# Performance work log

Hardware: AMD Instinct MI355X
Metric: run time of the kernel (lower is better)

## Reference

```python
import jax, jax.numpy as jnp
import numpy as np

N = 100000
E = 1600000
D = 64
N_LAYERS = 2


def setup_inputs() -> dict:
    key = jax.random.key(0)
    ks = jax.random.split(key, 4 + 4 * N_LAYERS)
    h = jax.random.normal(ks[0], (N, D), dtype=jnp.float32)
    x = jax.random.normal(ks[1], (N, 3), dtype=jnp.float32)
    edge_index = jax.random.randint(ks[2], (2, E), 0, N, dtype=jnp.int64)
    node_mask = jnp.ones((N, 1), dtype=jnp.float32)
    scale = 1.0 / np.sqrt(D)
    params = {}
    for i in range(N_LAYERS):
        params[f'W1_{i}'] = jax.random.normal(ks[4 + 4 * i], (D, D), dtype=jnp.float32) * scale
        params[f'b1_{i}'] = jax.random.normal(ks[5 + 4 * i], (D,), dtype=jnp.float32) * scale
        params[f'W2_{i}'] = jax.random.normal(ks[6 + 4 * i], (D, D), dtype=jnp.float32) * scale
        params[f'b2_{i}'] = jax.random.normal(ks[7 + 4 * i], (D,), dtype=jnp.float32) * scale
    return dict(h=h, x=x, edge_index=edge_index, node_mask=node_mask, **params)


def _gin_layer(h, src, dst, W1, b1, W2, b2):
    # GINConv with eps=0: mlp(h_i + sum_{j->i} h_j)
    agg = jax.ops.segment_sum(h[src], dst, num_segments=N)  # [N, D]
    z = h + agg
    z = jax.nn.relu(z @ W1 + b1)
    return z @ W2 + b2


def reference(h, x, edge_index, node_mask,
              W1_0, b1_0, W2_0, b2_0,
              W1_1, b1_1, W2_1, b2_1):
    src, dst = edge_index[0], edge_index[1]
    h = _gin_layer(h, src, dst, W1_0, b1_0, W2_0, b2_0)
    h = _gin_layer(h, src, dst, W1_1, b1_1, W2_1, b2_1)
    h = h * node_mask
    return (h, x)
```

## Files before the change

### kernel.cpp

```cpp
#include <hip/hip_runtime.h>


#define NN 100000
#define EE 1600000
#define CAP 48
#define NBIN 1024
#define CHB 6250
#define OVF_CAPN 8000

#define OVFC_OFF   1024
#define OVF_OFF    1026
#define BSTART_OFF 17056
#define CURSOR_OFF 18112
#define CNT_OFF    19200
#define BUCK_OFF   119296
#define BINNED_OFF 4919296
#define HB_OFF     4919296
#define PW_OFF     8119328

typedef __attribute__((ext_vector_type(8))) short s8v;
typedef __attribute__((ext_vector_type(4))) float f4v;

union U8 { unsigned u[4]; s8v s; };

static __device__ __forceinline__ unsigned short f2bf(float f) {
  unsigned u = __float_as_uint(f);
  return (unsigned short)((u + 0x7FFF + ((u >> 16) & 1)) >> 16);
}
static __device__ __forceinline__ float bf2f(unsigned short s) {
  return __uint_as_float(((unsigned)s) << 16);
}
static __device__ __forceinline__ unsigned pk2(float lo, float hi) {
  return (unsigned)f2bf(lo) | ((unsigned)f2bf(hi) << 16);
}

__global__ __launch_bounds__(256) void setup_k(const float* __restrict__ W1a,
                                               const float* __restrict__ W2a,
                                               const float* __restrict__ W1b,
                                               const float* __restrict__ W2b,
                                               unsigned short* __restrict__ pw,
                                               int* __restrict__ wsp) {
  const int t = threadIdx.x;
#pragma unroll
  for (int i = t; i < 2048; i += 256) wsp[i] = 0;
  const float* Ws[4] = {W1a, W2a, W1b, W2b};
#pragma unroll
  for (int m = 0; m < 4; ++m) {
    const float* __restrict__ W = Ws[m];
#pragma unroll 1
    for (int i = 0; i < 16; ++i) {
      const int e = i * 256 + t;
      const int j = e & 7;
      const int lv = (e >> 3) & 63;
      const int ks = (e >> 9) & 1;
      const int tt = e >> 10;
      const int k = ks * 32 + (lv >> 4) * 8 + j;
      const int n = tt * 16 + (lv & 15);
      pw[m * 4096 + e] = f2bf(W[k * 64 + n]);
    }
  }
}

__global__ __launch_bounds__(256) void hist_k(const int* __restrict__ dst,
                                              int* __restrict__ binTot) {
  __shared__ int hist[NBIN];
  const int t = threadIdx.x;
#pragma unroll
  for (int b = t; b < NBIN; b += 256) hist[b] = 0;
  __syncthreads();
  const int s = blockIdx.x * CHB;
#pragma unroll 1
  for (int p = t; p < CHB / 2; p += 256) {
    const int2 dd = *reinterpret_cast<const int2*>(dst + s + 2 * p);
    atomicAdd(&hist[dd.x >> 7], 1);
    atomicAdd(&hist[dd.y >> 7], 1);
  }
  __syncthreads();
#pragma unroll
  for (int b = t; b < NBIN; b += 256) {
    const int c = hist[b];
    if (c) atomicAdd(&binTot[b], c);
  }
}

__global__ __launch_bounds__(1024) void scan_k(const int* __restrict__ binTot,
                                               int* __restrict__ binStart,
                                               int* __restrict__ cursor) {
  __shared__ int sh[NBIN];
  const int t = threadIdx.x;
  const int v = binTot[t];
  sh[t] = v;
  __syncthreads();
  for (int off = 1; off < NBIN; off <<= 1) {
    const int x = (t >= off) ? sh[t - off] : 0;
    __syncthreads();
    sh[t] += x;
    __syncthreads();
  }
  binStart[t] = sh[t] - v;
  cursor[t] = sh[t] - v;
  if (t == NBIN - 1) binStart[NBIN] = sh[t];
}

__global__ __launch_bounds__(256) void scatter_k(const int* __restrict__ src,
                                                 const int* __restrict__ dst,
                                                 int* __restrict__ cursor,
                                                 int* __restrict__ binned) {
  __shared__ int hist[NBIN], base[NBIN], lcnt[NBIN];
  const int t = threadIdx.x;
#pragma unroll
  for (int b = t; b < NBIN; b += 256) { hist[b] = 0; lcnt[b] = 0; }
  __syncthreads();
  const int s = blockIdx.x * CHB;
#pragma unroll 1
  for (int p = t; p < CHB / 2; p += 256) {
    const int2 dd = *reinterpret_cast<const int2*>(dst + s + 2 * p);
    atomicAdd(&hist[dd.x >> 7], 1);
    atomicAdd(&hist[dd.y >> 7], 1);
  }
  __syncthreads();
#pragma unroll
  for (int b = t; b < NBIN; b += 256) {
    const int c = hist[b];
    base[b] = c ? atomicAdd(&cursor[b], c) : 0;
  }
  __syncthreads();
#pragma unroll 1
  for (int p = t; p < CHB / 2; p += 256) {
    const int i = s + 2 * p;
    const int2 dd = *reinterpret_cast<const int2*>(dst + i);
    const int2 ss = *reinterpret_cast<const int2*>(src + i);
    int bin = dd.x >> 7;
    int off = atomicAdd(&lcnt[bin], 1);
    binned[base[bin] + off] = ((dd.x & 127) << 17) | ss.x;
    bin = dd.y >> 7;
    off = atomicAdd(&lcnt[bin], 1);
    binned[base[bin] + off] = ((dd.y & 127) << 17) | ss.y;
  }
}

__global__ __launch_bounds__(256) void bucketize_k(const int* __restrict__ binStart,
                                                   const int* __restrict__ binned,
                                                   int* __restrict__ bucket,
                                                   int* __restrict__ cnt,
                                                   int* __restrict__ ovf) {
  __shared__ int c128[128];
  const int t = threadIdx.x;
  const int bin = blockIdx.x;
  const int nbase = bin << 7;
  if (t < 128) c128[t] = 0;
  __syncthreads();
  const int s0 = binStart[bin], s1 = binStart[bin + 1];
#pragma unroll 1
  for (int i = s0 + t; i < s1; i += 256) {
    const int p = binned[i];
    const int dlow = p >> 17;
    const int sv = p & 131071;
    const int slot = atomicAdd(&c128[dlow], 1);
    if (slot < CAP) {
      bucket[(nbase + dlow) * CAP + slot] = sv;
    } else {
      const int q = atomicAdd(&ovf[-2], 1);
      if (q < OVF_CAPN) { ovf[2 * q] = nbase + dlow; ovf[2 * q + 1] = sv; }
    }
  }
  __syncthreads();
  if (t < 128 && nbase + t < NN) {
    const int dc = min(c128[t], CAP);
    cnt[nbase + t] = c128[t];
    const int pad = min((dc + 15) & ~15, CAP);
    int* __restrict__ brow = bucket + (nbase + t) * CAP;
#pragma unroll 1
    for (int q2 = dc; q2 < pad; ++q2) brow[q2] = NN;
  }
}

__global__ __launch_bounds__(256) void cvtx_k(const float* __restrict__ h,
                                              unsigned* __restrict__ hb,
                                              const float* __restrict__ x,
                                              float* __restrict__ ox) {
  const int b = blockIdx.x;
  const int t = threadIdx.x;
  if (b < 3125) {
    const int i = b * 256 + t;
    const float4* __restrict__ h4 = reinterpret_cast<const float4*>(h);
    const float4 a = h4[2 * i], c = h4[2 * i + 1];
    uint4 o;
    o.x = pk2(a.x, a.y); o.y = pk2(a.z, a.w);
    o.z = pk2(c.x, c.y); o.w = pk2(c.z, c.w);
    reinterpret_cast<uint4*>(hb)[i] = o;
  } else {
    if (b == 3125 && t < 32) hb[NN * 32 + t] = 0;
    const int i = (b - 3125) * 256 + t;
    if (i < (NN * 3) / 4)
      reinterpret_cast<float4*>(ox)[i] = reinterpret_cast<const float4*>(x)[i];
  }
}

__global__ __launch_bounds__(256) void agg_k(const unsigned short* __restrict__ hb,
                                             const int* __restrict__ cnt,
                                             const int* __restrict__ bucket,
                                             unsigned* __restrict__ zbu) {
  const int l = threadIdx.x & 63;
  const int s = l >> 4, g = l & 15;
  int n = blockIdx.x * 4 + (threadIdx.x >> 6);
  n = __builtin_amdgcn_readfirstlane(n);
  if (n >= NN) return;
  const int deg = min(cnt[n], CAP);
  const int nit = (deg + 15) >> 4;
  const int4* __restrict__ brow4 = reinterpret_cast<const int4*>(bucket + n * CAP);
  const uint2* __restrict__ h2 = reinterpret_cast<const uint2*>(hb);

  const uint2 sv = h2[n * 16 + g];
  const unsigned m0 = (s == 0) ? sv.x : 0u;
  const unsigned m1 = (s == 0) ? sv.y : 0u;
  float a0 = __uint_as_float(m0 << 16);
  float a1 = __uint_as_float(m0 & 0xffff0000u);
  float a2 = __uint_as_float(m1 << 16);
  float a3 = __uint_as_float(m1 & 0xffff0000u);

#pragma unroll 1
  for (int it = 0; it < nit; ++it) {
    const int4 q = brow4[it * 4 + s];
    const uint2 v0 = h2[q.x * 16 + g];
    const uint2 v1 = h2[q.y * 16 + g];
    const uint2 v2 = h2[q.z * 16 + g];
    const uint2 v3 = h2[q.w * 16 + g];
#define ACCU(vv)                                   \
    a0 += __uint_as_float(vv.x << 16);             \
    a1 += __uint_as_float(vv.x & 0xffff0000u);     \
    a2 += __uint_as_float(vv.y << 16);             \
    a3 += __uint_as_float(vv.y & 0xffff0000u);
    ACCU(v0) ACCU(v1) ACCU(v2) ACCU(v3)
#undef ACCU
  }

  a0 += __shfl_xor(a0, 16); a1 += __shfl_xor(a1, 16);
  a2 += __shfl_xor(a2, 16); a3 += __shfl_xor(a3, 16);
  a0 += __shfl_xor(a0, 32); a1 += __shfl_xor(a1, 32);
  a2 += __shfl_xor(a2, 32); a3 += __shfl_xor(a3, 32);

  if (s == 0) {
    uint2 o;
    o.x = pk2(a0, a1);
    o.y = pk2(a2, a3);
    reinterpret_cast<uint2*>(zbu)[n * 32 + g] = o;
  }
}

__global__ __launch_bounds__(256) void ovf_fix_k(const unsigned short* __restrict__ hb,
                                                 char* __restrict__ zb,
                                                 const int* __restrict__ ovfCnt,
                                                 const int* __restrict__ ovf) {
  const int cv = min(ovfCnt[0], OVF_CAPN);
  const int l = threadIdx.x & 63;
  const int w = threadIdx.x >> 6;
  for (int p = w; p < cv; p += 4) {
    const int d = ovf[2 * p];
    const int s = ovf[2 * p + 1];
    const float add = bf2f(hb[(s << 6) | l]);
    unsigned* wp = reinterpret_cast<unsigned*>(zb + d * 256 + (l >> 1) * 4);
    const bool hi = l & 1;
    unsigned cur = atomicAdd(wp, 0u);
    while (true) {
      const unsigned short hv = hi ? (unsigned short)(cur >> 16) : (unsigned short)(cur & 0xffffu);
      const unsigned short nh = f2bf(bf2f(hv) + add);
      const unsigned nw = hi ? ((cur & 0x0000ffffu) | ((unsigned)nh << 16))
                             : ((cur & 0xffff0000u) | (unsigned)nh);
      const unsigned prev = atomicCAS(wp, cur, nw);
      if (prev == cur) break;
      cur = prev;
    }
  }
}

template <int OUTBF>
__global__ __launch_bounds__(256) void mlp_mfma_k(
    const char* __restrict__ zb,
    void* __restrict__ hout,
    const unsigned short* __restrict__ pw1, const float* __restrict__ b1,
    const unsigned short* __restrict__ pw2, const float* __restrict__ b2,
    const float* __restrict__ mask) {
  __shared__ unsigned ldsu[128 * 33];
  const int tid = threadIdx.x;
  const int w = tid >> 6, l = tid & 63, g = l >> 4, mi = l & 15;
  const int m0 = blockIdx.x * 128;
  const int rbase = w * 32;

  s8v zf[2][2];
#pragma unroll
  for (int tm = 0; tm < 2; ++tm) {
    const int node = m0 + rbase + tm * 16 + mi;
    const int nc = node < NN ? node : NN - 1;
#pragma unroll
    for (int ks = 0; ks < 2; ++ks)
      zf[tm][ks] = *reinterpret_cast<const s8v*>(zb + nc * 256 + (ks * 32 + g * 8) * 2);
  }

  f4v acc[4][2];
#pragma unroll
  for (int t = 0; t < 4; ++t) {
    const f4v bv = *reinterpret_cast<const f4v*>(b1 + t * 16 + g * 4);
    acc[t][0] = bv; acc[t][1] = bv;
  }
#pragma unroll
  for (int t = 0; t < 4; ++t) {
#pragma unroll
    for (int ks = 0; ks < 2; ++ks) {
      const s8v wf = *reinterpret_cast<const s8v*>(pw1 + ((t * 2 + ks) * 64 + l) * 8);
#pragma unroll
      for (int tm = 0; tm < 2; ++tm)
        acc[t][tm] = __builtin_amdgcn_mfma_f32_16x16x32_bf16(wf, zf[tm][ks], acc[t][tm], 0, 0, 0);
    }
  }

#pragma unroll
  for (int t = 0; t < 4; ++t) {
#pragma unroll
    for (int tm = 0; tm < 2; ++tm) {
      const f4v a = acc[t][tm];
      const int row = rbase + tm * 16 + mi;
      const int base = row * 33 + t * 8 + g * 2;
      ldsu[base]     = pk2(fmaxf(a.x, 0.f), fmaxf(a.y, 0.f));
      ldsu[base + 1] = pk2(fmaxf(a.z, 0.f), fmaxf(a.w, 0.f));
    }
  }
  __syncthreads();

  s8v cf[2][2];
#pragma unroll
  for (int tm = 0; tm < 2; ++tm) {
    const int row = rbase + tm * 16 + mi;
#pragma unroll
    for (int ks = 0; ks < 2; ++ks) {
      const int b0 = row * 33 + ks * 16 + g * 4;
      U8 u8;
      u8.u[0] = ldsu[b0 + 0];
      u8.u[1] = ldsu[b0 + 1];
      u8.u[2] = ldsu[b0 + 2];
      u8.u[3] = ldsu[b0 + 3];
      cf[tm][ks] = u8.s;
    }
  }

  f4v acc2[4][2];
#pragma unroll
  for (int t = 0; t < 4; ++t) {
    const f4v bv = *reinterpret_cast<const f4v*>(b2 + t * 16 + g * 4);
    acc2[t][0] = bv; acc2[t][1] = bv;
  }
#pragma unroll
  for (int t = 0; t < 4; ++t) {
#pragma unroll
    for (int ks = 0; ks < 2; ++ks) {
      const s8v wf = *reinterpret_cast<const s8v*>(pw2 + ((t * 2 + ks) * 64 + l) * 8);
#pragma unroll
      for (int tm = 0; tm < 2; ++tm)
        acc2[t][tm] = __builtin_amdgcn_mfma_f32_16x16x32_bf16(wf, cf[tm][ks], acc2[t][tm], 0, 0, 0);
    }
  }

  if (OUTBF) {
    unsigned* __restrict__ ho = reinterpret_cast<unsigned*>(hout);
#pragma unroll
    for (int tm = 0; tm < 2; ++tm) {
      const int node = m0 + rbase + tm * 16 + mi;
      if (node < NN) {
#pragma unroll
        for (int t = 0; t < 4; ++t) {
          const f4v a = acc2[t][tm];
          const int idx = node * 32 + t * 8 + g * 2;
          uint2 p;
          p.x = pk2(a.x, a.y);
          p.y = pk2(a.z, a.w);
          *reinterpret_cast<uint2*>(&ho[idx]) = p;
        }
      }
    }
  } else {
    float* __restrict__ fo = reinterpret_cast<float*>(hout);
#pragma unroll
    for (int tm = 0; tm < 2; ++tm) {
      const int node = m0 + rbase + tm * 16 + mi;
      if (node < NN) {
        const float mv = mask[node];
#pragma unroll
        for (int t = 0; t < 4; ++t) {
          f4v v = acc2[t][tm];
          v *= mv;
          *reinterpret_cast<f4v*>(fo + node * 64 + t * 16 + g * 4) = v;
        }
      }
    }
  }
}

extern "C" void kernel_launch(void* const* d_in, const int* in_sizes, int n_in,
                              void* d_out, int out_size, void* d_ws, size_t ws_size,
                              hipStream_t stream) {
  (void)in_sizes; (void)n_in; (void)out_size; (void)ws_size;
  const float* h    = (const float*)d_in[0];
  const float* x    = (const float*)d_in[1];
  const int*   ei   = (const int*)d_in[2];
  const float* mask = (const float*)d_in[3];
  const float* W1_0 = (const float*)d_in[4];
  const float* b1_0 = (const float*)d_in[5];
  const float* W2_0 = (const float*)d_in[6];
  const float* b2_0 = (const float*)d_in[7];
  const float* W1_1 = (const float*)d_in[8];
  const float* b1_1 = (const float*)d_in[9];
  const float* W2_1 = (const float*)d_in[10];
  const float* b2_1 = (const float*)d_in[11];
  float* out = (float*)d_out;

  const int* src = ei;
  const int* dst = ei + EE;

  int* wsp       = (int*)d_ws;
  int* binTot    = wsp;
  int* ovfCnt    = wsp + OVFC_OFF;
  int* ovf       = wsp + OVF_OFF;
  int* binStart  = wsp + BSTART_OFF;
  int* cursor    = wsp + CURSOR_OFF;
  int* cnt       = wsp + CNT_OFF;
  int* bucket    = wsp + BUCK_OFF;
  int* binned    = wsp + BINNED_OFF;
  unsigned* hb   = (unsigned*)(wsp + HB_OFF);
  unsigned short* pw = (unsigned short*)(wsp + PW_OFF);
  const unsigned short* hbs = (const unsigned short*)hb;
  unsigned* zbu  = (unsigned*)d_out;
  char* zb       = (char*)d_out;

  setup_k<<<1, 256, 0, stream>>>(W1_0, W2_0, W1_1, W2_1, pw, wsp);
  hist_k<<<256, 256, 0, stream>>>(dst, binTot);
  scan_k<<<1, 1024, 0, stream>>>(binTot, binStart, cursor);
  scatter_k<<<256, 256, 0, stream>>>(src, dst, cursor, binned);
  bucketize_k<<<782, 256, 0, stream>>>(binStart, binned, bucket, cnt, ovf);

  cvtx_k<<<3418, 256, 0, stream>>>(h, hb, x, out + NN * 64);

  agg_k<<<25000, 256, 0, stream>>>(hbs, cnt, bucket, zbu);
  ovf_fix_k<<<1, 256, 0, stream>>>(hbs, zb, ovfCnt, ovf);
  mlp_mfma_k<1><<<782, 256, 0, stream>>>(zb, hb, pw, b1_0, pw + 4096, b2_0, nullptr);

  agg_k<<<25000, 256, 0, stream>>>(hbs, cnt, bucket, zbu);
  ovf_fix_k<<<1, 256, 0, stream>>>(hbs, zb, ovfCnt, ovf);
  mlp_mfma_k<0><<<782, 256, 0, stream>>>(zb, out, pw + 8192, b1_1, pw + 12288, b2_1, mask);
}
```

Measured before the change: 164.4 us.

## Use fixed-capacity bins to drop histogram/scan passes; process two nodes per wave in aggregation

Edge binning now gives each destination bin a fixed-capacity region, so the separate histogram and scan kernels are removed. Edges that overflow a bin go to the existing overflow list. The aggregation kernel also handles two destination nodes per wavefront, which puts more independent gathers in flight and halves the grid size. The cost is extra register pressure, and correctness now depends on the overflow path whenever a bin exceeds its capacity.

Result: faster. 146.1 us (-11.1%).

```diff
diff --git a/kernel.cpp b/kernel.cpp
--- a/kernel.cpp
+++ b/kernel.cpp
@@ -5,13 +5,12 @@
 #define EE 1600000
 #define CAP 48
 #define NBIN 1024
+#define BINCAP 2688
 #define CHB 6250
 #define OVF_CAPN 8000
 
 #define OVFC_OFF   1024
 #define OVF_OFF    1026
-#define BSTART_OFF 17056
-#define CURSOR_OFF 18112
 #define CNT_OFF    19200
 #define BUCK_OFF   119296
 #define BINNED_OFF 4919296
@@ -42,7 +41,8 @@
                                                int* __restrict__ wsp) {
   const int t = threadIdx.x;
 #pragma unroll
-  for (int i = t; i < 2048; i += 256) wsp[i] = 0;
+  for (int i = t; i < NBIN; i += 256) wsp[i] = i * BINCAP;
+  if (t == 0) wsp[OVFC_OFF] = 0;
   const float* Ws[4] = {W1a, W2a, W1b, W2b};
 #pragma unroll
   for (int m = 0; m < 4; ++m) {
@@ -61,12 +61,15 @@
   }
 }
 
-__global__ __launch_bounds__(256) void hist_k(const int* __restrict__ dst,
-                                              int* __restrict__ binTot) {
-  __shared__ int hist[NBIN];
+__global__ __launch_bounds__(256) void scatter_k(const int* __restrict__ src,
+                                                 const int* __restrict__ dst,
+                                                 int* __restrict__ gcur,
+                                                 int* __restrict__ binned,
+                                                 int* __restrict__ ovf) {
+  __shared__ int hist[NBIN], base[NBIN], lcnt[NBIN];
   const int t = threadIdx.x;
 #pragma unroll
-  for (int b = t; b < NBIN; b += 256) hist[b] = 0;
+  for (int b = t; b < NBIN; b += 256) { hist[b] = 0; lcnt[b] = 0; }
   __syncthreads();
   const int s = blockIdx.x * CHB;
 #pragma unroll 1
@@ -79,50 +82,7 @@
 #pragma unroll
   for (int b = t; b < NBIN; b += 256) {
     const int c = hist[b];
-    if (c) atomicAdd(&binTot[b], c);
-  }
-}
-
-__global__ __launch_bounds__(1024) void scan_k(const int* __restrict__ binTot,
-                                               int* __restrict__ binStart,
-                                               int* __restrict__ cursor) {
-  __shared__ int sh[NBIN];
-  const int t = threadIdx.x;
-  const int v = binTot[t];
-  sh[t] = v;
-  __syncthreads();
-  for (int off = 1; off < NBIN; off <<= 1) {
-    const int x = (t >= off) ? sh[t - off] : 0;
-    __syncthreads();
-    sh[t] += x;
-    __syncthreads();
-  }
-  binStart[t] = sh[t] - v;
-  cursor[t] = sh[t] - v;
-  if (t == NBIN - 1) binStart[NBIN] = sh[t];
-}
-
-__global__ __launch_bounds__(256) void scatter_k(const int* __restrict__ src,
-                                                 const int* __restrict__ dst,
-                                                 int* __restrict__ cursor,
-                                                 int* __restrict__ binned) {
-  __shared__ int hist[NBIN], base[NBIN], lcnt[NBIN];
-  const int t = threadIdx.x;
-#pragma unroll
-  for (int b = t; b < NBIN; b += 256) { hist[b] = 0; lcnt[b] = 0; }
-  __syncthreads();
-  const int s = blockIdx.x * CHB;
-#pragma unroll 1
-  for (int p = t; p < CHB / 2; p += 256) {
-    const int2 dd = *reinterpret_cast<const int2*>(dst + s + 2 * p);
-    atomicAdd(&hist[dd.x >> 7], 1);
-    atomicAdd(&hist[dd.y >> 7], 1);
-  }
-  __syncthreads();
-#pragma unroll
-  for (int b = t; b < NBIN; b += 256) {
-    const int c = hist[b];
-    base[b] = c ? atomicAdd(&cursor[b], c) : 0;
+    base[b] = c ? atomicAdd(&gcur[b], c) : 0;
   }
   __syncthreads();
 #pragma unroll 1
@@ -130,16 +90,30 @@
     const int i = s + 2 * p;
     const int2 dd = *reinterpret_cast<const int2*>(dst + i);
     const int2 ss = *reinterpret_cast<const int2*>(src + i);
-    int bin = dd.x >> 7;
-    int off = atomicAdd(&lcnt[bin], 1);
-    binned[base[bin] + off] = ((dd.x & 127) << 17) | ss.x;
-    bin = dd.y >> 7;
-    off = atomicAdd(&lcnt[bin], 1);
-    binned[base[bin] + off] = ((dd.y & 127) << 17) | ss.y;
-  }
-}
-
-__global__ __launch_bounds__(256) void bucketize_k(const int* __restrict__ binStart,
+    {
+      const int bin = dd.x >> 7;
+      const int slot = base[bin] + atomicAdd(&lcnt[bin], 1);
+      if (slot < (bin + 1) * BINCAP) {
+        binned[slot] = ((dd.x & 127) << 17) | ss.x;
+      } else {
+        const int q = atomicAdd(&ovf[-2], 1);
+        if (q < OVF_CAPN) { ovf[2 * q] = dd.x; ovf[2 * q + 1] = ss.x; }
+      }
+    }
+    {
+      const int bin = dd.y >> 7;
+      const int slot = base[bin] + atomicAdd(&lcnt[bin], 1);
+      if (slot < (bin + 1) * BINCAP) {
+        binned[slot] = ((dd.y & 127) << 17) | ss.y;
+      } else {
+        const int q = atomicAdd(&ovf[-2], 1);
+        if (q < OVF_CAPN) { ovf[2 * q] = dd.y; ovf[2 * q + 1] = ss.y; }
+      }
+    }
+  }
+}
+
+__global__ __launch_bounds__(256) void bucketize_k(const int* __restrict__ gcur,
                                                    const int* __restrict__ binned,
                                                    int* __restrict__ bucket,
                                                    int* __restrict__ cnt,
@@ -150,7 +124,8 @@
   const int nbase = bin << 7;
   if (t < 128) c128[t] = 0;
   __syncthreads();
-  const int s0 = binStart[bin], s1 = binStart[bin + 1];
+  const int s0 = bin * BINCAP;
+  const int s1 = min(gcur[bin], s0 + BINCAP);
 #pragma unroll 1
   for (int i = s0 + t; i < s1; i += 256) {
     const int p = binned[i];
@@ -203,48 +178,90 @@
                                              unsigned* __restrict__ zbu) {
   const int l = threadIdx.x & 63;
   const int s = l >> 4, g = l & 15;
-  int n = blockIdx.x * 4 + (threadIdx.x >> 6);
-  n = __builtin_amdgcn_readfirstlane(n);
-  if (n >= NN) return;
-  const int deg = min(cnt[n], CAP);
-  const int nit = (deg + 15) >> 4;
-  const int4* __restrict__ brow4 = reinterpret_cast<const int4*>(bucket + n * CAP);
+  int nb = blockIdx.x * 8 + (threadIdx.x >> 6) * 2;
+  nb = __builtin_amdgcn_readfirstlane(nb);
+  const int n0 = nb, n1 = nb + 1;
+
+  const int2 c2 = *reinterpret_cast<const int2*>(cnt + n0);
+  const int deg0 = min(c2.x, CAP), deg1 = min(c2.y, CAP);
+  const int nit0 = (deg0 + 15) >> 4, nit1 = (deg1 + 15) >> 4;
+  const int nc = min(nit0, nit1);
+
+  const int4* __restrict__ br0 = reinterpret_cast<const int4*>(bucket + n0 * CAP);
+  const int4* __restrict__ br1 = reinterpret_cast<const int4*>(bucket + n1 * CAP);
   const uint2* __restrict__ h2 = reinterpret_cast<const uint2*>(hb);
 
-  const uint2 sv = h2[n * 16 + g];
-  const unsigned m0 = (s == 0) ? sv.x : 0u;
-  const unsigned m1 = (s == 0) ? sv.y : 0u;
-  float a0 = __uint_as_float(m0 << 16);
-  float a1 = __uint_as_float(m0 & 0xffff0000u);
-  float a2 = __uint_as_float(m1 << 16);
-  float a3 = __uint_as_float(m1 & 0xffff0000u);
-
-#pragma unroll 1
-  for (int it = 0; it < nit; ++it) {
-    const int4 q = brow4[it * 4 + s];
-    const uint2 v0 = h2[q.x * 16 + g];
-    const uint2 v1 = h2[q.y * 16 + g];
-    const uint2 v2 = h2[q.z * 16 + g];
-    const uint2 v3 = h2[q.w * 16 + g];
-#define ACCU(vv)                                   \
+  const uint2 sv0 = h2[n0 * 16 + g];
+  const uint2 sv1 = h2[n1 * 16 + g];
+  const unsigned p00 = (s == 0) ? sv0.x : 0u, p01 = (s == 0) ? sv0.y : 0u;
+  const unsigned p10 = (s == 0) ? sv1.x : 0u, p11 = (s == 0) ? sv1.y : 0u;
+  float a0 = __uint_as_float(p00 << 16), a1 = __uint_as_float(p00 & 0xffff0000u);
+  float a2 = __uint_as_float(p01 << 16), a3 = __uint_as_float(p01 & 0xffff0000u);
+  float b0 = __uint_as_float(p10 << 16), b1 = __uint_as_float(p10 & 0xffff0000u);
+  float b2 = __uint_as_float(p11 << 16), b3 = __uint_as_float(p11 & 0xffff0000u);
+
+#define ACCA(vv)                                   \
     a0 += __uint_as_float(vv.x << 16);             \
     a1 += __uint_as_float(vv.x & 0xffff0000u);     \
     a2 += __uint_as_float(vv.y << 16);             \
     a3 += __uint_as_float(vv.y & 0xffff0000u);
-    ACCU(v0) ACCU(v1) ACCU(v2) ACCU(v3)
-#undef ACCU
-  }
+#define ACCB(vv)                                   \
+    b0 += __uint_as_float(vv.x << 16);             \
+    b1 += __uint_as_float(vv.x & 0xffff0000u);     \
+    b2 += __uint_as_float(vv.y << 16);             \
+    b3 += __uint_as_float(vv.y & 0xffff0000u);
+
+#pragma unroll 1
+  for (int it = 0; it < nc; ++it) {
+    const int4 q0 = br0[it * 4 + s];
+    const int4 q1 = br1[it * 4 + s];
+    const uint2 v0 = h2[q0.x * 16 + g];
+    const uint2 v1 = h2[q0.y * 16 + g];
+    const uint2 v2 = h2[q0.z * 16 + g];
+    const uint2 v3 = h2[q0.w * 16 + g];
+    const uint2 w0 = h2[q1.x * 16 + g];
+    const uint2 w1 = h2[q1.y * 16 + g];
+    const uint2 w2 = h2[q1.z * 16 + g];
+    const uint2 w3 = h2[q1.w * 16 + g];
+    ACCA(v0) ACCA(v1) ACCA(v2) ACCA(v3)
+    ACCB(w0) ACCB(w1) ACCB(w2) ACCB(w3)
+  }
+#pragma unroll 1
+  for (int it = nc; it < nit0; ++it) {
+    const int4 q0 = br0[it * 4 + s];
+    const uint2 v0 = h2[q0.x * 16 + g];
+    const uint2 v1 = h2[q0.y * 16 + g];
+    const uint2 v2 = h2[q0.z * 16 + g];
+    const uint2 v3 = h2[q0.w * 16 + g];
+    ACCA(v0) ACCA(v1) ACCA(v2) ACCA(v3)
+  }
+#pragma unroll 1
+  for (int it = nc; it < nit1; ++it) {
+    const int4 q1 = br1[it * 4 + s];
+    const uint2 w0 = h2[q1.x * 16 + g];
+    const uint2 w1 = h2[q1.y * 16 + g];
+    const uint2 w2 = h2[q1.z * 16 + g];
+    const uint2 w3 = h2[q1.w * 16 + g];
+    ACCB(w0) ACCB(w1) ACCB(w2) ACCB(w3)
+  }
+#undef ACCA
+#undef ACCB
 
   a0 += __shfl_xor(a0, 16); a1 += __shfl_xor(a1, 16);
   a2 += __shfl_xor(a2, 16); a3 += __shfl_xor(a3, 16);
   a0 += __shfl_xor(a0, 32); a1 += __shfl_xor(a1, 32);
   a2 += __shfl_xor(a2, 32); a3 += __shfl_xor(a3, 32);
+  b0 += __shfl_xor(b0, 16); b1 += __shfl_xor(b1, 16);
+  b2 += __shfl_xor(b2, 16); b3 += __shfl_xor(b3, 16);
+  b0 += __shfl_xor(b0, 32); b1 += __shfl_xor(b1, 32);
+  b2 += __shfl_xor(b2, 32); b3 += __shfl_xor(b3, 32);
 
   if (s == 0) {
-    uint2 o;
-    o.x = pk2(a0, a1);
-    o.y = pk2(a2, a3);
-    reinterpret_cast<uint2*>(zbu)[n * 32 + g] = o;
+    uint2 o0, o1;
+    o0.x = pk2(a0, a1); o0.y = pk2(a2, a3);
+    o1.x = pk2(b0, b1); o1.y = pk2(b2, b3);
+    reinterpret_cast<uint2*>(zbu)[n0 * 32 + g] = o0;
+    reinterpret_cast<uint2*>(zbu)[n1 * 32 + g] = o1;
   }
 }
 
@@ -417,11 +434,9 @@
   const int* dst = ei + EE;
 
   int* wsp       = (int*)d_ws;
-  int* binTot    = wsp;
+  int* gcur      = wsp;
   int* ovfCnt    = wsp + OVFC_OFF;
   int* ovf       = wsp + OVF_OFF;
-  int* binStart  = wsp + BSTART_OFF;
-  int* cursor    = wsp + CURSOR_OFF;
   int* cnt       = wsp + CNT_OFF;
   int* bucket    = wsp + BUCK_OFF;
   int* binned    = wsp + BINNED_OFF;
@@ -432,18 +447,16 @@
   char* zb       = (char*)d_out;
 
   setup_k<<<1, 256, 0, stream>>>(W1_0, W2_0, W1_1, W2_1, pw, wsp);
-  hist_k<<<256, 256, 0, stream>>>(dst, binTot);
-  scan_k<<<1, 1024, 0, stream>>>(binTot, binStart, cursor);
-  scatter_k<<<256, 256, 0, stream>>>(src, dst, cursor, binned);
-  bucketize_k<<<782, 256, 0, stream>>>(binStart, binned, bucket, cnt, ovf);
+  scatter_k<<<256, 256, 0, stream>>>(src, dst, gcur, binned, ovf);
+  bucketize_k<<<782, 256, 0, stream>>>(gcur, binned, bucket, cnt, ovf);
 
   cvtx_k<<<3418, 256, 0, stream>>>(h, hb, x, out + NN * 64);
 
-  agg_k<<<25000, 256, 0, stream>>>(hbs, cnt, bucket, zbu);
+  agg_k<<<12500, 256, 0, stream>>>(hbs, cnt, bucket, zbu);
   ovf_fix_k<<<1, 256, 0, stream>>>(hbs, zb, ovfCnt, ovf);
   mlp_mfma_k<1><<<782, 256, 0, stream>>>(zb, hb, pw, b1_0, pw + 4096, b2_0, nullptr);
 
-  agg_k<<<25000, 256, 0, stream>>>(hbs, cnt, bucket, zbu);
+  agg_k<<<12500, 256, 0, stream>>>(hbs, cnt, bucket, zbu);
   ovf_fix_k<<<1, 256, 0, stream>>>(hbs, zb, ovfCnt, ovf);
   mlp_mfma_k<0><<<782, 256, 0, stream>>>(zb, out, pw + 8192, b1_1, pw + 12288, b2_1, mask);
 }
```
